# Kernel tuning notes

Measured on AMD Instinct MI355X. Metric: run time of the kernel, lower is better.

## Reference

```python
import jax, jax.numpy as jnp
import numpy as np

V, D, M, C, L = 100000, 256, 4096, 4096, 32
PAD = 0
EPS = 1e-8  # torch CosineSimilarity default eps


def setup_inputs() -> dict:
    key = jax.random.key(0)
    ks = jax.random.split(key, 6)
    xs = jax.random.randint(ks[0], (1, L), 0, V)
    mems = jax.random.randint(ks[1], (M, L), 0, V)
    ys = jax.random.randint(ks[2], (1, L), 0, V)
    cands = jax.random.randint(ks[3], (C, L), 0, V)
    lt = jax.random.normal(ks[4], (V, D), dtype=jnp.float32) * 0.02
    lt = lt.at[PAD].set(0.0)  # nn.Embedding padding_idx row is zero
    freqs = jax.random.uniform(ks[5], (V,), dtype=jnp.float32, minval=0.05, maxval=1.0)
    return {"xs": xs, "mems": mems, "ys": ys, "cands": cands, "lt": lt, "freqs": freqs}


def _encode(tokens, lt, freqs):
    # Batched Encoder.forward: freq-weighted average of token embeddings.
    # tokens: [N, L] -> [N, D]
    emb = lt[tokens]                       # [N, L, D] gather
    w = freqs[tokens]                      # [N, L]
    w = w / jnp.linalg.norm(w, axis=1, keepdims=True)  # w * (1 / ||w||)
    return jnp.einsum('nl,nld->nd', w, emb)


def reference(xs, mems, ys, cands, lt, freqs):
    xs_emb = _encode(xs, lt, freqs)                                   # [1, D]
    mems_enc = jnp.concatenate([_encode(mems, lt, freqs), xs_emb], 0)  # [M+1, D]
    # cosine similarity of xs_emb (broadcast) against each memory row
    an = jnp.maximum(jnp.linalg.norm(xs_emb, axis=1), EPS)            # [1]
    bn = jnp.maximum(jnp.linalg.norm(mems_enc, axis=1), EPS)          # [M+1]
    cos = (mems_enc @ xs_emb[0]) / (an * bn)                          # [M+1]
    att = jax.nn.softmax(cos)[None, :]                                # [1, M+1]
    lhs_emb = att @ mems_enc                                          # [1, D]
    ys_emb = _encode(ys, lt, freqs)                                   # [1, D]
    cand_emb = _encode(cands, lt, freqs)                              # [C, D]
    # torch.cat of lhs_emb repeated (1 + C) times; ys then cand encodings
    xs_out = jnp.tile(lhs_emb, (cands.shape[0] + 1, 1))               # [C+1, D]
    ys_out = jnp.concatenate([ys_emb, cand_emb], axis=0)              # [C+1, D]
    return xs_out, ys_out
```

## Files before the change

kernel.cpp:

```cpp
#include <hip/hip_runtime.h>

#define V_ 100000
#define D_ 256
#define M_ 4096
#define C_ 4096
#define L_ 32
#define ROWS_MEMS (M_ + 1)
#define NTASK (1 + M_ + 1 + C_)
#define NBLK 1025
#define HALF (NBLK * 4)
#define NV4 ((V_ * D_) / 4)

__device__ __forceinline__ float wave_allreduce_sum(float v) {
    #pragma unroll
    for (int off = 32; off >= 1; off >>= 1) v += __shfl_xor(v, off, 64);
    return v;
}

__device__ __forceinline__ float half_allreduce_sum(float v) {
    #pragma unroll
    for (int off = 16; off >= 1; off >>= 1) v += __shfl_xor(v, off, 64);
    return v;
}

__device__ __forceinline__ unsigned short f2bf_rne(float f) {
    unsigned int u = __float_as_uint(f);
    u += 0x7FFFu + ((u >> 16) & 1u);
    return (unsigned short)(u >> 16);
}
__device__ __forceinline__ float bf2f(unsigned short b) {
    return __uint_as_float((unsigned int)b << 16);
}

__global__ __launch_bounds__(256) void convert_lt(
    const float4* __restrict__ lt4, ushort4* __restrict__ bt4)
{
    const int i = blockIdx.x * 256 + threadIdx.x;
    if (i >= NV4) return;
    const float4 v = lt4[i];
    ushort4 o;
    o.x = f2bf_rne(v.x); o.y = f2bf_rne(v.y);
    o.z = f2bf_rne(v.z); o.w = f2bf_rne(v.w);
    bt4[i] = o;
}

__global__ __launch_bounds__(256) void encode_fused(
    const int* __restrict__ xs, const int* __restrict__ mems,
    const int* __restrict__ ys, const int* __restrict__ cands,
    const unsigned short* __restrict__ bt,
    const float* __restrict__ freqs,
    float* __restrict__ lhs_raw,
    float* __restrict__ gsum,
    float* __restrict__ out_ys)
{
    __shared__ float s_xf[D_];
    __shared__ float s_lred[D_];
    __shared__ float s_an2, s_ered;

    const int wave = threadIdx.x >> 6;
    const int lane = threadIdx.x & 63;
    const int d0 = lane * 4;
    const int g = blockIdx.x * 4 + wave;

    s_lred[threadIdx.x] = 0.f;
    if (threadIdx.x == 0) s_ered = 0.f;

    if (wave == 0) {
        int txs = 0; float wxs = 0.f;
        if (lane < L_) { txs = xs[lane]; wxs = freqs[txs]; }
        const float sx2 = wave_allreduce_sum(wxs * wxs);
        const float wnx = wxs / sqrtf(sx2);
        float4 xf = make_float4(0.f, 0.f, 0.f, 0.f);
        #pragma unroll
        for (int l = 0; l < L_; ++l) {
            const int t = __shfl(txs, l, 64);
            const float wl = __shfl(wnx, l, 64);
            const ushort4 b = *reinterpret_cast<const ushort4*>(bt + (size_t)t * D_ + d0);
            xf.x += wl * bf2f(b.x); xf.y += wl * bf2f(b.y);
            xf.z += wl * bf2f(b.z); xf.w += wl * bf2f(b.w);
        }
        *reinterpret_cast<float4*>(&s_xf[d0]) = xf;
        const float an2 = wave_allreduce_sum(xf.x*xf.x + xf.y*xf.y + xf.z*xf.z + xf.w*xf.w);
        if (lane == 0) s_an2 = an2;
    }
    __syncthreads();

    const int rtA = g;
    const int* tpA; float* dstA = nullptr; int aiA = -1;
    if (rtA == 0) {
        tpA = xs; aiA = M_;
    } else if (rtA <= M_) {
        tpA = mems + (size_t)(rtA - 1) * L_; aiA = rtA - 1;
    } else if (rtA == M_ + 1) {
        tpA = ys; dstA = out_ys;
    } else {
        const int c = rtA - (M_ + 2);
        tpA = cands + (size_t)c * L_;
        dstA = out_ys + (size_t)(c + 1) * D_;
    }

    const int rtB = g + HALF;
    const bool hasB = (rtB < NTASK);
    const int cB = hasB ? (rtB - (M_ + 2)) : 0;
    const int* tpB = cands + (size_t)cB * L_;
    float* dstB = out_ys + (size_t)(cB + 1) * D_;

    const int tok = (lane < 32) ? tpA[lane] : tpB[lane - 32];
    const float w = freqs[tok];
    const float s2 = half_allreduce_sum(w * w);
    const float wn = w / sqrtf(s2);

    float4 accA = make_float4(0.f, 0.f, 0.f, 0.f);
    float4 accB = make_float4(0.f, 0.f, 0.f, 0.f);
    #pragma unroll
    for (int l = 0; l < L_; ++l) {
        const int   ta = __shfl(tok, l, 64);
        const int   tb = __shfl(tok, 32 + l, 64);
        const float wa = __shfl(wn, l, 64);
        const float wb = __shfl(wn, 32 + l, 64);
        const ushort4 ba = *reinterpret_cast<const ushort4*>(bt + (size_t)ta * D_ + d0);
        const ushort4 bb = *reinterpret_cast<const ushort4*>(bt + (size_t)tb * D_ + d0);
        accA.x += wa * bf2f(ba.x); accA.y += wa * bf2f(ba.y);
        accA.z += wa * bf2f(ba.z); accA.w += wa * bf2f(ba.w);
        accB.x += wb * bf2f(bb.x); accB.y += wb * bf2f(bb.y);
        accB.z += wb * bf2f(bb.z); accB.w += wb * bf2f(bb.w);
    }

    if (aiA >= 0) {
        const float4 xf = *reinterpret_cast<const float4*>(&s_xf[d0]);
        const float d = wave_allreduce_sum(accA.x*xf.x + accA.y*xf.y + accA.z*xf.z + accA.w*xf.w);
        const float q = wave_allreduce_sum(accA.x*accA.x + accA.y*accA.y + accA.z*accA.z + accA.w*accA.w);
        const float an = fmaxf(sqrtf(s_an2), 1e-8f);
        const float bn = fmaxf(sqrtf(q),  1e-8f);
        const float e = expf(d / (an * bn));
        atomicAdd(&s_lred[d0 + 0], e * accA.x);
        atomicAdd(&s_lred[d0 + 1], e * accA.y);
        atomicAdd(&s_lred[d0 + 2], e * accA.z);
        atomicAdd(&s_lred[d0 + 3], e * accA.w);
        if (lane == 0) atomicAdd(&s_ered, e);
    } else {
        *reinterpret_cast<float4*>(dstA + d0) = accA;
    }
    if (hasB) *reinterpret_cast<float4*>(dstB + d0) = accB;

    __syncthreads();
    atomicAdd(&lhs_raw[threadIdx.x], s_lred[threadIdx.x]);
    if (threadIdx.x == 0) atomicAdd(gsum, s_ered);
}

__global__ __launch_bounds__(256) void finalize_tile(
    const float* __restrict__ lhs_raw, const float* __restrict__ gsum,
    float* __restrict__ out_xs)
{
    const float val = lhs_raw[threadIdx.x] / gsum[0];
    for (int r = blockIdx.x; r < ROWS_MEMS; r += gridDim.x)
        out_xs[(size_t)r * D_ + threadIdx.x] = val;
}

extern "C" void kernel_launch(void* const* d_in, const int* in_sizes, int n_in,
                              void* d_out, int out_size, void* d_ws, size_t ws_size,
                              hipStream_t stream) {
    const int*   xs    = (const int*)d_in[0];
    const int*   mems  = (const int*)d_in[1];
    const int*   ys    = (const int*)d_in[2];
    const int*   cands = (const int*)d_in[3];
    const float* lt    = (const float*)d_in[4];
    const float* freqs = (const float*)d_in[5];

    float* out    = (float*)d_out;
    float* out_xs = out;
    float* out_ys = out + (size_t)ROWS_MEMS * D_;

    unsigned short* bt = (unsigned short*)d_ws;
    float* lhs_raw = (float*)(bt + (size_t)V_ * D_);
    float* gsum    = lhs_raw + D_;

    hipMemsetAsync(lhs_raw, 0, (D_ + 1) * sizeof(float), stream);

    convert_lt<<<(NV4 + 255) / 256, 256, 0, stream>>>(
        (const float4*)lt, (ushort4*)bt);
    encode_fused<<<NBLK, 256, 0, stream>>>(xs, mems, ys, cands, bt, freqs,
                                           lhs_raw, gsum, out_ys);
    finalize_tile<<<1024, 256, 0, stream>>>(lhs_raw, gsum, out_xs);
}
```

Measured before the change: 209.3 us.

## Use one row per wave with 16-byte bf16 loads split across half-waves

Each wave now encodes a single row instead of two. The two half-waves each take alternate tokens and load 8 bf16 values with one 16-byte load, then combine their partial sums with a cross-half shuffle. The grid grows to cover all tasks one per wave. Non-attention blocks skip the x-encoding and the global atomic reduction. This trades fewer rows in flight per wave for wider loads and less shuffle work per token, which may lower memory-level parallelism per wave in a gather-bound kernel.

Measured after the change: 212.2 us. About the same (+1.4%).

```diff
diff --git a/kernel.cpp b/kernel.cpp
--- a/kernel.cpp
+++ b/kernel.cpp
@@ -7,8 +7,6 @@
 #define L_ 32
 #define ROWS_MEMS (M_ + 1)
 #define NTASK (1 + M_ + 1 + C_)
-#define NBLK 1025
-#define HALF (NBLK * 4)
 #define NV4 ((V_ * D_) / 4)
 
 __device__ __forceinline__ float wave_allreduce_sum(float v) {
@@ -17,19 +15,10 @@
     return v;
 }
 
-__device__ __forceinline__ float half_allreduce_sum(float v) {
-    #pragma unroll
-    for (int off = 16; off >= 1; off >>= 1) v += __shfl_xor(v, off, 64);
-    return v;
-}
-
 __device__ __forceinline__ unsigned short f2bf_rne(float f) {
     unsigned int u = __float_as_uint(f);
     u += 0x7FFFu + ((u >> 16) & 1u);
     return (unsigned short)(u >> 16);
-}
-__device__ __forceinline__ float bf2f(unsigned short b) {
-    return __uint_as_float((unsigned int)b << 16);
 }
 
 __global__ __launch_bounds__(256) void convert_lt(
@@ -59,93 +48,117 @@
 
     const int wave = threadIdx.x >> 6;
     const int lane = threadIdx.x & 63;
-    const int d0 = lane * 4;
-    const int g = blockIdx.x * 4 + wave;
+    const int sub  = lane >> 5;
+    const int dlo  = (lane & 31) * 8;
+    const int rt = blockIdx.x * 4 + wave;
+    const bool valid = (rt < NTASK);
+    const bool batt = (blockIdx.x <= M_ / 4);
 
     s_lred[threadIdx.x] = 0.f;
     if (threadIdx.x == 0) s_ered = 0.f;
 
-    if (wave == 0) {
-        int txs = 0; float wxs = 0.f;
-        if (lane < L_) { txs = xs[lane]; wxs = freqs[txs]; }
-        const float sx2 = wave_allreduce_sum(wxs * wxs);
-        const float wnx = wxs / sqrtf(sx2);
-        float4 xf = make_float4(0.f, 0.f, 0.f, 0.f);
+    if (batt && wave == 0) {
+        int tokx = 0; float wx = 0.f;
+        if (lane < L_) { tokx = xs[lane]; wx = freqs[tokx]; }
+        const float sx2 = wave_allreduce_sum(wx * wx);
+        const float wnx = wx / sqrtf(sx2);
+        float xa[8];
         #pragma unroll
-        for (int l = 0; l < L_; ++l) {
-            const int t = __shfl(txs, l, 64);
-            const float wl = __shfl(wnx, l, 64);
-            const ushort4 b = *reinterpret_cast<const ushort4*>(bt + (size_t)t * D_ + d0);
-            xf.x += wl * bf2f(b.x); xf.y += wl * bf2f(b.y);
-            xf.z += wl * bf2f(b.z); xf.w += wl * bf2f(b.w);
+        for (int j = 0; j < 8; ++j) xa[j] = 0.f;
+        #pragma unroll
+        for (int l = 0; l < L_ / 2; ++l) {
+            const int   idx = 2 * l + sub;
+            const int   t  = __shfl(tokx, idx, 64);
+            const float wl = __shfl(wnx,  idx, 64);
+            const uint4 p = *reinterpret_cast<const uint4*>(bt + (size_t)t * D_ + dlo);
+            xa[0] += wl * __uint_as_float(p.x << 16);
+            xa[1] += wl * __uint_as_float(p.x & 0xFFFF0000u);
+            xa[2] += wl * __uint_as_float(p.y << 16);
+            xa[3] += wl * __uint_as_float(p.y & 0xFFFF0000u);
+            xa[4] += wl * __uint_as_float(p.z << 16);
+            xa[5] += wl * __uint_as_float(p.z & 0xFFFF0000u);
+            xa[6] += wl * __uint_as_float(p.w << 16);
+            xa[7] += wl * __uint_as_float(p.w & 0xFFFF0000u);
         }
-        *reinterpret_cast<float4*>(&s_xf[d0]) = xf;
-        const float an2 = wave_allreduce_sum(xf.x*xf.x + xf.y*xf.y + xf.z*xf.z + xf.w*xf.w);
+        #pragma unroll
+        for (int j = 0; j < 8; ++j) xa[j] += __shfl_xor(xa[j], 32, 64);
+        #pragma unroll
+        for (int j = 0; j < 4; ++j) s_xf[dlo + sub * 4 + j] = xa[sub * 4 + j];
+        float pq = 0.f;
+        #pragma unroll
+        for (int j = 0; j < 8; ++j) pq += xa[j] * xa[j];
+        const float an2 = wave_allreduce_sum(pq) * 0.5f;
         if (lane == 0) s_an2 = an2;
     }
     __syncthreads();
 
-    const int rtA = g;
-    const int* tpA; float* dstA = nullptr; int aiA = -1;
-    if (rtA == 0) {
-        tpA = xs; aiA = M_;
-    } else if (rtA <= M_) {
-        tpA = mems + (size_t)(rtA - 1) * L_; aiA = rtA - 1;
-    } else if (rtA == M_ + 1) {
-        tpA = ys; dstA = out_ys;
-    } else {
-        const int c = rtA - (M_ + 2);
-        tpA = cands + (size_t)c * L_;
-        dstA = out_ys + (size_t)(c + 1) * D_;
+    const int* tok_ptr = cands; float* dst = nullptr; int ai = -1;
+    if (valid) {
+        if (rt == 0)           { tok_ptr = xs; ai = M_; }
+        else if (rt <= M_)     { tok_ptr = mems + (size_t)(rt - 1) * L_; ai = rt - 1; }
+        else if (rt == M_ + 1) { tok_ptr = ys; dst = out_ys; }
+        else {
+            const int c = rt - (M_ + 2);
+            tok_ptr = cands + (size_t)c * L_;
+            dst = out_ys + (size_t)(c + 1) * D_;
+        }
     }
 
-    const int rtB = g + HALF;
-    const bool hasB = (rtB < NTASK);
-    const int cB = hasB ? (rtB - (M_ + 2)) : 0;
-    const int* tpB = cands + (size_t)cB * L_;
-    float* dstB = out_ys + (size_t)(cB + 1) * D_;
-
-    const int tok = (lane < 32) ? tpA[lane] : tpB[lane - 32];
-    const float w = freqs[tok];
-    const float s2 = half_allreduce_sum(w * w);
+    int tok = 0; float w = 0.f;
+    if (valid && lane < L_) { tok = tok_ptr[lane]; w = freqs[tok]; }
+    const float s2 = wave_allreduce_sum(w * w);
     const float wn = w / sqrtf(s2);
 
-    float4 accA = make_float4(0.f, 0.f, 0.f, 0.f);
-    float4 accB = make_float4(0.f, 0.f, 0.f, 0.f);
+    float acc[8];
     #pragma unroll
-    for (int l = 0; l < L_; ++l) {
-        const int   ta = __shfl(tok, l, 64);
-        const int   tb = __shfl(tok, 32 + l, 64);
-        const float wa = __shfl(wn, l, 64);
-        const float wb = __shfl(wn, 32 + l, 64);
-        const ushort4 ba = *reinterpret_cast<const ushort4*>(bt + (size_t)ta * D_ + d0);
-        const ushort4 bb = *reinterpret_cast<const ushort4*>(bt + (size_t)tb * D_ + d0);
-        accA.x += wa * bf2f(ba.x); accA.y += wa * bf2f(ba.y);
-        accA.z += wa * bf2f(ba.z); accA.w += wa * bf2f(ba.w);
-        accB.x += wb * bf2f(bb.x); accB.y += wb * bf2f(bb.y);
-        accB.z += wb * bf2f(bb.z); accB.w += wb * bf2f(bb.w);
+    for (int j = 0; j < 8; ++j) acc[j] = 0.f;
+    if (valid) {
+        #pragma unroll
+        for (int l = 0; l < L_ / 2; ++l) {
+            const int   idx = 2 * l + sub;
+            const int   t  = __shfl(tok, idx, 64);
+            const float wl = __shfl(wn,  idx, 64);
+            const uint4 p = *reinterpret_cast<const uint4*>(bt + (size_t)t * D_ + dlo);
+            acc[0] += wl * __uint_as_float(p.x << 16);
+            acc[1] += wl * __uint_as_float(p.x & 0xFFFF0000u);
+            acc[2] += wl * __uint_as_float(p.y << 16);
+            acc[3] += wl * __uint_as_float(p.y & 0xFFFF0000u);
+            acc[4] += wl * __uint_as_float(p.z << 16);
+            acc[5] += wl * __uint_as_float(p.z & 0xFFFF0000u);
+            acc[6] += wl * __uint_as_float(p.w << 16);
+            acc[7] += wl * __uint_as_float(p.w & 0xFFFF0000u);
+        }
+        #pragma unroll
+        for (int j = 0; j < 8; ++j) acc[j] += __shfl_xor(acc[j], 32, 64);
+
+        if (ai >= 0) {
+            float pd = 0.f, pq = 0.f;
+            #pragma unroll
+            for (int j = 0; j < 8; ++j) {
+                pd += acc[j] * s_xf[dlo + j];
+                pq += acc[j] * acc[j];
+            }
+            const float d = wave_allreduce_sum(pd) * 0.5f;
+            const float q = wave_allreduce_sum(pq) * 0.5f;
+            const float an = fmaxf(sqrtf(s_an2), 1e-8f);
+            const float bn = fmaxf(sqrtf(q),  1e-8f);
+            const float e = expf(d / (an * bn));
+            #pragma unroll
+            for (int j = 0; j < 4; ++j)
+                atomicAdd(&s_lred[dlo + sub * 4 + j], e * acc[sub * 4 + j]);
+            if (lane == 0) atomicAdd(&s_ered, e);
+        } else {
+            const float4 st = make_float4(acc[sub * 4 + 0], acc[sub * 4 + 1],
+                                          acc[sub * 4 + 2], acc[sub * 4 + 3]);
+            *reinterpret_cast<float4*>(dst + dlo + sub * 4) = st;
+        }
     }
 
-    if (aiA >= 0) {
-        const float4 xf = *reinterpret_cast<const float4*>(&s_xf[d0]);
-        const float d = wave_allreduce_sum(accA.x*xf.x + accA.y*xf.y + accA.z*xf.z + accA.w*xf.w);
-        const float q = wave_allreduce_sum(accA.x*accA.x + accA.y*accA.y + accA.z*accA.z + accA.w*accA.w);
-        const float an = fmaxf(sqrtf(s_an2), 1e-8f);
-        const float bn = fmaxf(sqrtf(q),  1e-8f);
-        const float e = expf(d / (an * bn));
-        atomicAdd(&s_lred[d0 + 0], e * accA.x);
-        atomicAdd(&s_lred[d0 + 1], e * accA.y);
-        atomicAdd(&s_lred[d0 + 2], e * accA.z);
-        atomicAdd(&s_lred[d0 + 3], e * accA.w);
-        if (lane == 0) atomicAdd(&s_ered, e);
-    } else {
-        *reinterpret_cast<float4*>(dstA + d0) = accA;
+    if (batt) {
+        __syncthreads();
+        atomicAdd(&lhs_raw[threadIdx.x], s_lred[threadIdx.x]);
+        if (threadIdx.x == 0) atomicAdd(gsum, s_ered);
     }
-    if (hasB) *reinterpret_cast<float4*>(dstB + d0) = accB;
-
-    __syncthreads();
-    atomicAdd(&lhs_raw[threadIdx.x], s_lred[threadIdx.x]);
-    if (threadIdx.x == 0) atomicAdd(gsum, s_ered);
 }
 
 __global__ __launch_bounds__(256) void finalize_tile(
@@ -179,7 +192,7 @@
 
     convert_lt<<<(NV4 + 255) / 256, 256, 0, stream>>>(
         (const float4*)lt, (ushort4*)bt);
-    encode_fused<<<NBLK, 256, 0, stream>>>(xs, mems, ys, cands, bt, freqs,
-                                           lhs_raw, gsum, out_ys);
+    encode_fused<<<(NTASK + 3) / 4, 256, 0, stream>>>(xs, mems, ys, cands, bt, freqs,
+                                                      lhs_raw, gsum, out_ys);
     finalize_tile<<<1024, 256, 0, stream>>>(lhs_raw, gsum, out_xs);
 }
```
